# Kernel tuning notes

Measured on AMD Instinct MI355X. Metric: run time of the kernel, lower is better.

Reference implementation:

```python
import jax, jax.numpy as jnp
import numpy as np

T, N, H = 16384, 512, 512
R_MIN, R_MAX = 0.9, 0.999
MAX_PHASE = float(np.pi) / 10


def setup_inputs() -> dict:
    key = jax.random.key(0)
    ks = jax.random.split(key, 10)
    x = jax.random.normal(ks[0], (T, H), dtype=jnp.float32)
    # theta_init: log(max_phase * u1)
    u1 = jax.random.uniform(ks[1], (N,))
    theta_log = jnp.log(MAX_PHASE * u1).astype(jnp.float32)
    # nu_init: log(-0.5 * log(u * (r_max^2 - r_min^2) + r_min^2))
    u2 = jax.random.uniform(ks[2], (N,))
    nu_log = jnp.log(-0.5 * jnp.log(u2 * (R_MAX ** 2 - R_MIN ** 2) + R_MIN ** 2)).astype(jnp.float32)
    B_re = jax.random.normal(ks[3], (N, H), dtype=jnp.float32) / jnp.sqrt(2.0 * H)
    B_im = jax.random.normal(ks[4], (N, H), dtype=jnp.float32) / jnp.sqrt(2.0 * H)
    C_re = jax.random.normal(ks[5], (H, N), dtype=jnp.float32) / jnp.sqrt(1.0 * N)
    C_im = jax.random.normal(ks[6], (H, N), dtype=jnp.float32) / jnp.sqrt(1.0 * N)
    C_re2 = jax.random.normal(ks[7], (H, N), dtype=jnp.float32) / jnp.sqrt(1.0 * N)
    C_im2 = jax.random.normal(ks[8], (H, N), dtype=jnp.float32) / jnp.sqrt(1.0 * N)
    D = jax.random.normal(ks[9], (H,), dtype=jnp.float32)
    return {"x": x, "theta_log": theta_log, "nu_log": nu_log,
            "B_re": B_re, "B_im": B_im, "C_re": C_re, "C_im": C_im,
            "C_re2": C_re2, "C_im2": C_im2, "D": D}


def _binop(ei, ej):
    a_i, bu_i = ei
    a_j, bu_j = ej
    return (a_j * a_i, a_j * bu_i + bu_j)


def reference(x, theta_log, nu_log, B_re, B_im, C_re, C_im, C_re2, C_im2, D):
    # Lambda: complex diagonal transition, |Lambda| < 1
    Lambda = jnp.exp(-jnp.exp(nu_log) + 1j * jnp.exp(theta_log))  # (N,) complex
    gamma = jnp.sqrt(1.0 - jnp.abs(Lambda) ** 2)                  # (N,)
    B_norm = (B_re + 1j * B_im) * gamma[:, None]                  # (N, H) complex
    L = x.shape[0]
    Lambda_elements = jnp.repeat(Lambda[None, :], L, axis=0)      # (L, N)
    Bu = jnp.einsum('LH,NH->LN', x + 0j, B_norm)                  # (L, N) complex
    _, fwd_states = jax.lax.associative_scan(_binop, (Lambda_elements, Bu))
    _, bwd_states = jax.lax.associative_scan(_binop, (Lambda_elements, Bu), reverse=True)
    C = jnp.concatenate([C_re + 1j * C_im, C_re2 + 1j * C_im2], axis=-1)   # (H, 2N)
    states = jnp.concatenate([fwd_states, bwd_states], axis=-1)            # (L, 2N)
    y = jnp.einsum('HN,LN->LH', C, states).real + D[None, :] * x
    return y
```

## Files before the change

kernel.cpp:

```cpp
#include <hip/hip_runtime.h>
#include <hip/hip_bf16.h>
#include <cstdint>
#include <cstddef>


#define L_DIM 16384
#define N_DIM 512
#define H_DIM 512
#define CH    64
#define NCH   256

typedef short s16x8 __attribute__((ext_vector_type(8)));
typedef float f32x4 __attribute__((ext_vector_type(4)));

__device__ inline void split2(float v, unsigned short* hi, unsigned short* lo) {
    __hip_bfloat16 h = __float2bfloat16(v);
    float hv = __bfloat162float(h);
    __hip_bfloat16 l = __float2bfloat16(v - hv);
    *hi = *(unsigned short*)&h;
    *lo = *(unsigned short*)&l;
}

__device__ inline void split_store2(float a, float b,
                                    unsigned short* hp, unsigned short* lp) {
    unsigned short ha, la, hb, lb;
    split2(a, &ha, &la);
    split2(b, &hb, &lb);
    *(unsigned int*)hp = (unsigned int)ha | ((unsigned int)hb << 16);
    *(unsigned int*)lp = (unsigned int)la | ((unsigned int)lb << 16);
}

__device__ inline void gload16(const void* g, void* l) {
    __builtin_amdgcn_global_load_lds(
        (const __attribute__((address_space(1))) void*)g,
        (__attribute__((address_space(3))) void*)l, 16, 0, 0);
}

__device__ inline void lam_of(int n, const float* nu_log, const float* th_log,
                              float& lr, float& li) {
    float nu = expf(nu_log[n]);
    float th = expf(th_log[n]);
    float em = expf(-nu);
    lr = em * cosf(th);
    li = em * sinf(th);
}

__global__ void k_convert(const float* __restrict__ x,
                          const float* __restrict__ Bre, const float* __restrict__ Bim,
                          const float* __restrict__ Cre, const float* __restrict__ Cim,
                          const float* __restrict__ Cre2, const float* __restrict__ Cim2,
                          const float* __restrict__ nu_log, const float* __restrict__ th_log,
                          unsigned short* __restrict__ xh, unsigned short* __restrict__ xl,
                          unsigned short* __restrict__ bnh, unsigned short* __restrict__ bnl,
                          unsigned short* __restrict__ cch, unsigned short* __restrict__ ccl)
{
    const int XU = L_DIM * H_DIM / 4;
    const int BU = 2 * N_DIM * H_DIM / 4;
    const int CU = 4 * H_DIM * N_DIM / 4;
    const int TOT = XU + BU + CU;
    for (int u = blockIdx.x * blockDim.x + threadIdx.x; u < TOT;
         u += gridDim.x * blockDim.x) {
        if (u < XU) {
            int i0 = u * 4;
            float4 v = *(const float4*)(x + i0);
            split2(v.x, xh + i0 + 0, xl + i0 + 0);
            split2(v.y, xh + i0 + 1, xl + i0 + 1);
            split2(v.z, xh + i0 + 2, xl + i0 + 2);
            split2(v.w, xh + i0 + 3, xl + i0 + 3);
        } else if (u < XU + BU) {
            int i0 = (u - XU) * 4;
            int row = i0 >> 9;
            int h0  = i0 & 511;
            int n   = row & (N_DIM - 1);
            const float* src = (row < N_DIM) ? Bre : Bim;
            float nu = expf(nu_log[n]);
            float g  = sqrtf(fmaxf(0.f, 1.f - expf(-2.f * nu)));
            float4 v = *(const float4*)(src + n * H_DIM + h0);
            split2(g * v.x, bnh + i0 + 0, bnl + i0 + 0);
            split2(g * v.y, bnh + i0 + 1, bnl + i0 + 1);
            split2(g * v.z, bnh + i0 + 2, bnl + i0 + 2);
            split2(g * v.w, bnh + i0 + 3, bnl + i0 + 3);
        } else {
            int i0 = (u - XU - BU) * 4;
            int h   = i0 >> 11;
            int k0  = i0 & 2047;
            int mat = k0 >> 9;
            int c0  = k0 & 511;
            const float* src = (mat == 0) ? Cre : (mat == 1) ? Cim
                             : (mat == 2) ? Cre2 : Cim2;
            float s = (mat & 1) ? -1.f : 1.f;
            float4 v = *(const float4*)(src + h * N_DIM + c0);
            split2(s * v.x, cch + i0 + 0, ccl + i0 + 0);
            split2(s * v.y, cch + i0 + 1, ccl + i0 + 1);
            split2(s * v.z, cch + i0 + 2, ccl + i0 + 2);
            split2(s * v.w, cch + i0 + 3, ccl + i0 + 3);
        }
    }
}

template<bool EPI, int K, int NC>
__global__ __launch_bounds__(256, 2)
void k_gemm(const unsigned short* __restrict__ Ah, const unsigned short* __restrict__ Al,
            const unsigned short* __restrict__ Bh, const unsigned short* __restrict__ Bl,
            float* __restrict__ Out,
            const float* __restrict__ Dv, const float* __restrict__ Xres)
{
    __shared__ unsigned short smem[4 * 128 * 32];
    const int tid  = threadIdx.x;
    const int wave = tid >> 6;
    const int lane = tid & 63;

    constexpr int GX = NC / 128;
    const int nwg  = GX * (L_DIM / 128);
    const int flat = blockIdx.y * GX + blockIdx.x;
    const int q    = nwg >> 3;
    const int nf   = (flat & 7) * q + (flat >> 3);
    const int brow = (nf / GX) * 128;
    const int bcol = (nf % GX) * 128;

    const int wr   = wave >> 1;
    const int wc   = wave & 1;

    const unsigned short* gsrc = (wave == 0) ? Ah : (wave == 1) ? Al
                               : (wave == 2) ? Bh : Bl;
    const int rowbase = (wave < 2) ? brow : bcol;
    const unsigned short* gp = gsrc
        + (size_t)(rowbase + (lane >> 2)) * K
        + (((lane & 3) ^ ((lane >> 3) & 3)) << 3);
    unsigned short* lbase = smem + wave * 4096;

    f32x4 acc[4][4];
    #pragma unroll
    for (int i = 0; i < 4; ++i) {
        #pragma unroll
        for (int j = 0; j < 4; ++j) acc[i][j] = (f32x4){0.f, 0.f, 0.f, 0.f};
    }

    const int r    = lane & 15;
    const int kg   = lane >> 4;
    const int slot = ((kg ^ ((r >> 1) & 3)) << 3);

    const unsigned short* sAh = smem;
    const unsigned short* sAl = smem + 4096;
    const unsigned short* sBh = smem + 8192;
    const unsigned short* sBl = smem + 12288;

    const int nK = K >> 5;
    for (int kt = 0; kt < nK; ++kt) {
        const unsigned short* g = gp + kt * 32;
        #pragma unroll
        for (int j = 0; j < 8; ++j)
            gload16(g + (size_t)j * 16 * K, lbase + j * 512);
        __syncthreads();

        s16x8 ah[4], al[4];
        #pragma unroll
        for (int mi = 0; mi < 4; ++mi) {
            int row = wr * 64 + mi * 16 + r;
            ah[mi] = *(const s16x8*)(sAh + row * 32 + slot);
            al[mi] = *(const s16x8*)(sAl + row * 32 + slot);
        }
        #pragma unroll
        for (int ni = 0; ni < 4; ++ni) {
            int rowb = wc * 64 + ni * 16 + r;
            s16x8 bh = *(const s16x8*)(sBh + rowb * 32 + slot);
            s16x8 bl = *(const s16x8*)(sBl + rowb * 32 + slot);
            #pragma unroll
            for (int mi = 0; mi < 4; ++mi) {
                acc[mi][ni] = __builtin_amdgcn_mfma_f32_16x16x32_bf16(ah[mi], bh, acc[mi][ni], 0, 0, 0);
                acc[mi][ni] = __builtin_amdgcn_mfma_f32_16x16x32_bf16(al[mi], bh, acc[mi][ni], 0, 0, 0);
                acc[mi][ni] = __builtin_amdgcn_mfma_f32_16x16x32_bf16(ah[mi], bl, acc[mi][ni], 0, 0, 0);
            }
        }
        __syncthreads();
    }

    #pragma unroll
    for (int mi = 0; mi < 4; ++mi) {
        #pragma unroll
        for (int ni = 0; ni < 4; ++ni) {
            #pragma unroll
            for (int j = 0; j < 4; ++j) {
                int row = brow + wr * 64 + mi * 16 + kg * 4 + j;
                int col = bcol + wc * 64 + ni * 16 + r;
                float v = acc[mi][ni][j];
                if (EPI) v += Dv[col] * Xres[(size_t)row * H_DIM + col];
                Out[(size_t)row * NC + col] = v;
            }
        }
    }
}

__global__ void k_scan1(const float* __restrict__ Bu,
                        const float* __restrict__ nu_log, const float* __restrict__ th_log,
                        float* __restrict__ cfr, float* __restrict__ cfi,
                        float* __restrict__ cbr, float* __restrict__ cbi)
{
    const int n = threadIdx.x;
    const int c = blockIdx.x;
    float lr, li; lam_of(n, nu_log, th_log, lr, li);
    float sfr = 0.f, sfi = 0.f, sbr = 0.f, sbi = 0.f, pr = 1.f, pi = 0.f;
    const float* base = Bu + (size_t)c * CH * 1024;
    for (int l = 0; l < CH; ++l) {
        float ur = base[l * 1024 + n];
        float ui = base[l * 1024 + 512 + n];
        float tr = lr * sfr - li * sfi + ur;
        float ti = lr * sfi + li * sfr + ui;
        sfr = tr; sfi = ti;
        sbr += pr * ur - pi * ui;
        sbi += pr * ui + pi * ur;
        float t2 = lr * pr - li * pi;
        pi = lr * pi + li * pr;
        pr = t2;
    }
    int o = c * N_DIM + n;
    cfr[o] = sfr; cfi[o] = sfi; cbr[o] = sbr; cbi[o] = sbi;
}

__global__ void k_scan2(const float* __restrict__ nu_log, const float* __restrict__ th_log,
                        float* __restrict__ cfr, float* __restrict__ cfi,
                        float* __restrict__ cbr, float* __restrict__ cbi)
{
    const int n = threadIdx.x;
    float nu = expf(nu_log[n]);
    float th = expf(th_log[n]);
    float mg = expf(-(float)CH * nu);
    float ph = (float)CH * th;
    float Pr = mg * cosf(ph);
    float Pi = mg * sinf(ph);
    if (blockIdx.x == 0) {
        float ar = 0.f, ai = 0.f;
        for (int c = 0; c < NCH; ++c) {
            int o = c * N_DIM + n;
            float tr = cfr[o], ti = cfi[o];
            cfr[o] = ar; cfi[o] = ai;
            float nr  = tr + Pr * ar - Pi * ai;
            float ni_ = ti + Pr * ai + Pi * ar;
            ar = nr; ai = ni_;
        }
    } else {
        float ar = 0.f, ai = 0.f;
        for (int c = NCH - 1; c >= 0; --c) {
            int o = c * N_DIM + n;
            float tr = cbr[o], ti = cbi[o];
            cbr[o] = ar; cbi[o] = ai;
            float nr  = tr + Pr * ar - Pi * ai;
            float ni_ = ti + Pr * ai + Pi * ar;
            ar = nr; ai = ni_;
        }
    }
}

__global__ void k_scan3(const float* __restrict__ Bu,
                        const float* __restrict__ nu_log, const float* __restrict__ th_log,
                        const float* __restrict__ cfr, const float* __restrict__ cfi,
                        const float* __restrict__ cbr, const float* __restrict__ cbi,
                        unsigned short* __restrict__ Sh, unsigned short* __restrict__ Sl)
{
    const int t  = threadIdx.x;
    const int c  = blockIdx.x;
    const int n0 = 2 * t;
    const int n1 = 2 * t + 1;
    float lr0, li0, lr1, li1;
    lam_of(n0, nu_log, th_log, lr0, li0);
    lam_of(n1, nu_log, th_log, lr1, li1);
    const float* base = Bu + (size_t)c * CH * 1024;
    unsigned short* shb = Sh + (size_t)c * CH * 2048;
    unsigned short* slb = Sl + (size_t)c * CH * 2048;
    const int o0 = c * N_DIM + n0;
    const int o1 = c * N_DIM + n1;

    float sr0 = cfr[o0], si0 = cfi[o0];
    float sr1 = cfr[o1], si1 = cfi[o1];
    for (int l = 0; l < CH; ++l) {
        float2 ur = *(const float2*)(base + l * 1024 + n0);
        float2 ui = *(const float2*)(base + l * 1024 + 512 + n0);
        float tr0 = lr0 * sr0 - li0 * si0 + ur.x;
        float ti0 = lr0 * si0 + li0 * sr0 + ui.x;
        sr0 = tr0; si0 = ti0;
        float tr1 = lr1 * sr1 - li1 * si1 + ur.y;
        float ti1 = lr1 * si1 + li1 * sr1 + ui.y;
        sr1 = tr1; si1 = ti1;
        split_store2(sr0, sr1, shb + l * 2048 + n0,       slb + l * 2048 + n0);
        split_store2(si0, si1, shb + l * 2048 + 512 + n0, slb + l * 2048 + 512 + n0);
    }
    sr0 = cbr[o0]; si0 = cbi[o0];
    sr1 = cbr[o1]; si1 = cbi[o1];
    for (int l = CH - 1; l >= 0; --l) {
        float2 ur = *(const float2*)(base + l * 1024 + n0);
        float2 ui = *(const float2*)(base + l * 1024 + 512 + n0);
        float tr0 = lr0 * sr0 - li0 * si0 + ur.x;
        float ti0 = lr0 * si0 + li0 * sr0 + ui.x;
        sr0 = tr0; si0 = ti0;
        float tr1 = lr1 * sr1 - li1 * si1 + ur.y;
        float ti1 = lr1 * si1 + li1 * sr1 + ui.y;
        sr1 = tr1; si1 = ti1;
        split_store2(sr0, sr1, shb + l * 2048 + 1024 + n0, slb + l * 2048 + 1024 + n0);
        split_store2(si0, si1, shb + l * 2048 + 1536 + n0, slb + l * 2048 + 1536 + n0);
    }
}

extern "C" void kernel_launch(void* const* d_in, const int* in_sizes, int n_in,
                              void* d_out, int out_size, void* d_ws, size_t ws_size,
                              hipStream_t stream)
{
    const float* x      = (const float*)d_in[0];
    const float* th_log = (const float*)d_in[1];
    const float* nu_log = (const float*)d_in[2];
    const float* Bre    = (const float*)d_in[3];
    const float* Bim    = (const float*)d_in[4];
    const float* Cre    = (const float*)d_in[5];
    const float* Cim    = (const float*)d_in[6];
    const float* Cre2   = (const float*)d_in[7];
    const float* Cim2   = (const float*)d_in[8];
    const float* Dv     = (const float*)d_in[9];
    float* y = (float*)d_out;

    char* ws = (char*)d_ws;
    const size_t MB = 1048576;
    float*          Bu  = (float*)         (ws + 0);
    unsigned short* cch = (unsigned short*)(ws + 64 * MB);
    unsigned short* ccl = (unsigned short*)(ws + 66 * MB);
    float*          cfr = (float*)         (ws + 68 * MB);
    float*          cfi = cfr + NCH * N_DIM;
    float*          cbr = cfi + NCH * N_DIM;
    float*          cbi = cbr + NCH * N_DIM;
    unsigned short* Sh  = (unsigned short*)(ws + 70 * MB);
    unsigned short* Sl  = (unsigned short*)(ws + 134 * MB);
    unsigned short* xh  = (unsigned short*)(ws + 70 * MB);
    unsigned short* xl  = (unsigned short*)(ws + 86 * MB);
    unsigned short* bnh = (unsigned short*)(ws + 102 * MB);
    unsigned short* bnl = (unsigned short*)(ws + 103 * MB);
    if (ws_size < (size_t)198 * MB) return;

    k_convert<<<dim3(2048), dim3(256), 0, stream>>>(
        x, Bre, Bim, Cre, Cim, Cre2, Cim2, nu_log, th_log,
        xh, xl, bnh, bnl, cch, ccl);

    k_gemm<false, 512, 1024><<<dim3(8, 128), dim3(256), 0, stream>>>(
        xh, xl, bnh, bnl, Bu, nullptr, nullptr);

    k_scan1<<<dim3(NCH), dim3(512), 0, stream>>>(
        Bu, nu_log, th_log, cfr, cfi, cbr, cbi);

    k_scan2<<<dim3(2), dim3(512), 0, stream>>>(
        nu_log, th_log, cfr, cfi, cbr, cbi);

    k_scan3<<<dim3(NCH), dim3(256), 0, stream>>>(
        Bu, nu_log, th_log, cfr, cfi, cbr, cbi, Sh, Sl);

    k_gemm<true, 2048, 512><<<dim3(4, 128), dim3(256), 0, stream>>>(
        Sh, Sl, cch, ccl, y, Dv, x);
}
```

Baseline: 337.9 us.

## Parallelize chunk-carry scan with wave-level shuffle prefix scan

The middle scan stage, which propagates carries across 256 chunks, used to run on only 2 blocks with one thread per state, each walking sequentially through all chunks. It now gives each (direction, state) pair its own wavefront. Each lane handles 4 chunks locally and a Kogge-Stone prefix scan over complex affine pairs using shuffles combines them, launched on 256 blocks. This removes a long serial dependency chain on a nearly idle GPU, at the cost of strided uncoalesced global accesses and slightly different floating-point rounding order.

```diff
diff --git a/kernel.cpp b/kernel.cpp
--- a/kernel.cpp
+++ b/kernel.cpp
@@ -221,32 +221,76 @@
                         float* __restrict__ cfr, float* __restrict__ cfi,
                         float* __restrict__ cbr, float* __restrict__ cbi)
 {
-    const int n = threadIdx.x;
+    const int wave_id = blockIdx.x * (blockDim.x >> 6) + (threadIdx.x >> 6);
+    const int lane    = threadIdx.x & 63;
+    const int dir     = wave_id >> 9;
+    const int n       = wave_id & 511;
+
     float nu = expf(nu_log[n]);
     float th = expf(th_log[n]);
     float mg = expf(-(float)CH * nu);
     float ph = (float)CH * th;
-    float Pr = mg * cosf(ph);
-    float Pi = mg * sinf(ph);
-    if (blockIdx.x == 0) {
-        float ar = 0.f, ai = 0.f;
-        for (int c = 0; c < NCH; ++c) {
-            int o = c * N_DIM + n;
-            float tr = cfr[o], ti = cfi[o];
-            cfr[o] = ar; cfi[o] = ai;
-            float nr  = tr + Pr * ar - Pi * ai;
-            float ni_ = ti + Pr * ai + Pi * ar;
-            ar = nr; ai = ni_;
-        }
-    } else {
-        float ar = 0.f, ai = 0.f;
-        for (int c = NCH - 1; c >= 0; --c) {
-            int o = c * N_DIM + n;
-            float tr = cbr[o], ti = cbi[o];
-            cbr[o] = ar; cbi[o] = ai;
-            float nr  = tr + Pr * ar - Pi * ai;
-            float ni_ = ti + Pr * ai + Pi * ar;
-            ar = nr; ai = ni_;
+    float Pcr = mg * cosf(ph);
+    float Pci = mg * sinf(ph);
+
+    float* Vr = dir ? cbr : cfr;
+    float* Vi = dir ? cbi : cfi;
+
+    int c0 = 4 * lane;
+    int idx[4];
+    #pragma unroll
+    for (int j = 0; j < 4; ++j) {
+        int pos = c0 + j;
+        int c   = dir ? (NCH - 1 - pos) : pos;
+        idx[j] = c * N_DIM + n;
+    }
+    float vr[4], vi[4];
+    #pragma unroll
+    for (int j = 0; j < 4; ++j) { vr[j] = Vr[idx[j]]; vi[j] = Vi[idx[j]]; }
+
+    float p_r[4], p_i[4];
+    p_r[0] = 0.f; p_i[0] = 0.f;
+    #pragma unroll
+    for (int j = 0; j < 3; ++j) {
+        p_r[j + 1] = vr[j] + Pcr * p_r[j] - Pci * p_i[j];
+        p_i[j + 1] = vi[j] + Pcr * p_i[j] + Pci * p_r[j];
+    }
+    float Ir = vr[3] + Pcr * p_r[3] - Pci * p_i[3];
+    float Ii = vi[3] + Pcr * p_i[3] + Pci * p_r[3];
+    float P2r = Pcr * Pcr - Pci * Pci,  P2i = 2.f * Pcr * Pci;
+    float P3r = P2r * Pcr - P2i * Pci,  P3i = P2r * Pci + P2i * Pcr;
+    float Ar  = P3r * Pcr - P3i * Pci,  Ai  = P3r * Pci + P3i * Pcr;
+
+    #pragma unroll
+    for (int s = 1; s < 64; s <<= 1) {
+        float Irp = __shfl_up(Ir, (unsigned)s, 64);
+        float Iip = __shfl_up(Ii, (unsigned)s, 64);
+        float Arp = __shfl_up(Ar, (unsigned)s, 64);
+        float Aip = __shfl_up(Ai, (unsigned)s, 64);
+        if (lane >= s) {
+            float nIr = Ar * Irp - Ai * Iip + Ir;
+            float nIi = Ar * Iip + Ai * Irp + Ii;
+            Ir = nIr; Ii = nIi;
+            float nAr = Ar * Arp - Ai * Aip;
+            float nAi = Ar * Aip + Ai * Arp;
+            Ar = nAr; Ai = nAi;
+        }
+    }
+    float Lr = __shfl_up(Ir, 1u, 64);
+    float Li = __shfl_up(Ii, 1u, 64);
+    if (lane == 0) { Lr = 0.f; Li = 0.f; }
+
+    float Pjr = 1.f, Pji = 0.f;
+    #pragma unroll
+    for (int j = 0; j < 4; ++j) {
+        float cr = p_r[j] + Pjr * Lr - Pji * Li;
+        float ci = p_i[j] + Pjr * Li + Pji * Lr;
+        Vr[idx[j]] = cr;
+        Vi[idx[j]] = ci;
+        if (j < 3) {
+            float t = Pjr * Pcr - Pji * Pci;
+            Pji = Pjr * Pci + Pji * Pcr;
+            Pjr = t;
         }
     }
 }
@@ -343,7 +387,7 @@
     k_scan1<<<dim3(NCH), dim3(512), 0, stream>>>(
         Bu, nu_log, th_log, cfr, cfi, cbr, cbi);
 
-    k_scan2<<<dim3(2), dim3(512), 0, stream>>>(
+    k_scan2<<<dim3(256), dim3(256), 0, stream>>>(
         nu_log, th_log, cfr, cfi, cbr, cbi);
 
     k_scan3<<<dim3(NCH), dim3(256), 0, stream>>>(
```

New measurement: 322.6 us. 4.5% less time.
